# Optimization experiments

Hardware: AMD Instinct MI355X
Metric: run time of the kernel (lower is better)

Reference implementation:

```python
import jax, jax.numpy as jnp
import numpy as np

HID = 1024
HEADS = 16
HEAD_DIM = HID // HEADS
PF = 4096
EPS = 1e-5


def _linear_params(key, d_in, d_out):
    kw, kb = jax.random.split(key)
    bound = 1.0 / np.sqrt(d_in)
    W = jax.random.uniform(kw, (d_in, d_out), jnp.float32, -bound, bound)
    b = jax.random.uniform(kb, (d_out,), jnp.float32, -bound, bound)
    return W, b


def setup_inputs() -> dict:
    key = jax.random.key(0)
    ks = jax.random.split(key, 8)
    src = jax.random.normal(ks[0], (4, 2048, HID), jnp.float32)
    src_mask = jnp.ones((4, 1, 1, 2048), jnp.int32)
    Wq, bq = _linear_params(ks[1], HID, HID)
    Wk, bk = _linear_params(ks[2], HID, HID)
    Wv, bv = _linear_params(ks[3], HID, HID)
    Wo, bo = _linear_params(ks[4], HID, HID)
    W1, b1 = _linear_params(ks[5], HID, PF)
    W2, b2 = _linear_params(ks[6], PF, HID)
    ln1_g = jnp.ones((HID,), jnp.float32); ln1_b = jnp.zeros((HID,), jnp.float32)
    ln2_g = jnp.ones((HID,), jnp.float32); ln2_b = jnp.zeros((HID,), jnp.float32)
    return dict(src=src, src_mask=src_mask, Wq=Wq, bq=bq, Wk=Wk, bk=bk,
                Wv=Wv, bv=bv, Wo=Wo, bo=bo, W1=W1, b1=b1, W2=W2, b2=b2,
                ln1_g=ln1_g, ln1_b=ln1_b, ln2_g=ln2_g, ln2_b=ln2_b)


def _layernorm(x, g, b):
    mu = jnp.mean(x, axis=-1, keepdims=True)
    var = jnp.mean(jnp.square(x - mu), axis=-1, keepdims=True)
    return (x - mu) * jax.lax.rsqrt(var + EPS) * g + b


def _forward(src, src_mask, Wq, bq, Wk, bk, Wv, bv, Wo, bo,
             W1, b1, W2, b2, ln1_g, ln1_b, ln2_g, ln2_b):
    B, S, _ = src.shape
    # multi-head attention
    Q = (src @ Wq + bq).reshape(B, S, HEADS, HEAD_DIM)
    K = (src @ Wk + bk).reshape(B, S, HEADS, HEAD_DIM)
    V = (src @ Wv + bv).reshape(B, S, HEADS, HEAD_DIM)
    scale = np.sqrt(HEAD_DIM).astype(np.float32)
    energy = jnp.einsum('bqnh,bknh->bnqk', Q, K) / scale
    energy = jnp.where(src_mask == 0, jnp.float32(-1e10), energy)
    attn = jax.nn.softmax(energy, axis=-1)
    x = jnp.einsum('bnqk,bknh->bqnh', attn, V).reshape(B, S, HID)
    x = x @ Wo + bo
    src = _layernorm(src + x, ln1_g, ln1_b)
    # feedforward (swish)
    h = src @ W1 + b1
    h = h * jax.nn.sigmoid(h)
    h = h @ W2 + b2
    return _layernorm(src + h, ln2_g, ln2_b)


def reference(src, src_mask, Wq, bq, Wk, bk, Wv, bv, Wo, bo,
              W1, b1, W2, b2, ln1_g, ln1_b, ln2_g, ln2_b):
    return _forward(src, src_mask, Wq, bq, Wk, bk, Wv, bv, Wo, bo,
                    W1, b1, W2, b2, ln1_g, ln1_b, ln2_g, ln2_b)
```

## Files before the change

kernel.cpp:

```cpp
#include <hip/hip_runtime.h>
#include <stdint.h>


typedef __bf16 bf16;
typedef __bf16 bf16x4 __attribute__((ext_vector_type(4)));
typedef __bf16 bf16x8 __attribute__((ext_vector_type(8)));
typedef float  f32x4  __attribute__((ext_vector_type(4)));

__device__ __forceinline__ bf16 f2b(float x){
  uint32_t u = __builtin_bit_cast(uint32_t, x);
  uint32_t r = (u + 0x7FFFu + ((u >> 16) & 1u)) >> 16;
  return __builtin_bit_cast(bf16, (uint16_t)r);
}

__device__ __forceinline__ float ex2(float x){
#if __has_builtin(__builtin_amdgcn_exp2f)
  return __builtin_amdgcn_exp2f(x);
#else
  return __exp2f(x);
#endif
}

__device__ __forceinline__ void gload_lds16(const void* g, void* l){
  __builtin_amdgcn_global_load_lds(
      (const __attribute__((address_space(1))) void*)g,
      (__attribute__((address_space(3))) void*)l, 16, 0, 0);
}

__global__ __launch_bounds__(256) void prep_kernel(
    const float* __restrict__ src, bf16* __restrict__ srcb,
    const float* __restrict__ Wq, const float* __restrict__ Wk,
    const float* __restrict__ Wv, const float* __restrict__ Wo,
    const float* __restrict__ W1, const float* __restrict__ W2,
    bf16* __restrict__ Wqkvt, bf16* __restrict__ Wot,
    bf16* __restrict__ W1t,  bf16* __restrict__ W2t)
{
  __shared__ float t[32][33];
  const int bb = blockIdx.x, tid = threadIdx.x;
  if (bb < 8192){
    const int i = bb*256 + tid;
    const float4 v = ((const float4*)src)[i];
    bf16x4 u = { f2b(v.x), f2b(v.y), f2b(v.z), f2b(v.w) };
    *(bf16x4*)(srcb + (size_t)i*4) = u;
    return;
  }
  const int idx = bb - 8192;
  const float* W; bf16* Wt; int K, N, bx, by;
  if (idx < 3072){
    const int r = idx >> 10, j = idx & 1023;
    W = (r==0)?Wq:(r==1)?Wk:Wv; Wt = Wqkvt + (size_t)r*1024*1024;
    K = 1024; N = 1024; bx = j & 31; by = j >> 5;
  } else if (idx < 4096){
    const int j = idx - 3072;
    W = Wo; Wt = Wot; K = 1024; N = 1024; bx = j & 31; by = j >> 5;
  } else if (idx < 8192){
    const int j = idx - 4096;
    W = W1; Wt = W1t; K = 1024; N = 4096; bx = j & 127; by = j >> 7;
  } else {
    const int j = idx - 8192;
    W = W2; Wt = W2t; K = 4096; N = 1024; bx = j & 31; by = j >> 5;
  }
  const int x = tid & 31, y = tid >> 5;
  const int n0 = bx*32, k0 = by*32;
  #pragma unroll
  for (int r=0;r<4;r++) t[y+8*r][x] = W[(size_t)(k0+y+8*r)*N + n0+x];
  __syncthreads();
  #pragma unroll
  for (int r=0;r<4;r++) Wt[(size_t)(n0+y+8*r)*K + k0+x] = f2b(t[x][y+8*r]);
}

template<int OMODE, int REMAP>
__global__ __launch_bounds__(256) void gemm_bt_kernel(
    const bf16* __restrict__ A, const bf16* __restrict__ Bt,
    const float* __restrict__ bias, void* __restrict__ C,
    int M, int N, int K, float oscale,
    const float* __restrict__ bias2, const float* __restrict__ bias3,
    void* __restrict__ C2, void* __restrict__ C3)
{
  __shared__ bf16 As[2][128*64];
  __shared__ bf16 Bs[2][128*64];
  const int tid = threadIdx.x;
  const int w = tid >> 6, lane = tid & 63;
  const int wr = w >> 1, wc = w & 1;
  const int g16 = lane >> 4, l16 = lane & 15;

  const int nbx = N >> 7;
  const int nby = M >> 7;
  const int lin = blockIdx.x;
  int bx, by;
  if constexpr (REMAP==1){
    const int xcd = lin & 7;
    const int j   = lin >> 3;
    by = xcd * (nby >> 3) + (j / nbx);
    bx = j % nbx;
  } else {
    bx = lin % nbx;
    by = lin / nbx;
  }
  const int m0 = by*128, n0 = bx*128;

  const int srow  = tid >> 3;
  const int sslot = ((tid & 7) ^ (srow & 7)) * 8;
  const bf16* gA = A  + (size_t)(m0 + srow)*K + sslot;
  const bf16* gB = Bt + (size_t)(n0 + srow)*K + sslot;

  f32x4 acc[4][4];
  const f32x4 fz = {0.f,0.f,0.f,0.f};
  #pragma unroll
  for (int m=0;m<4;m++)
    #pragma unroll
    for (int n=0;n<4;n++) acc[m][n] = fz;

  bf16x8 ra[4], rb[4];
  #pragma unroll
  for (int k=0;k<4;k++){
    ra[k] = *(const bf16x8*)(gA + (size_t)(32*k)*K);
    rb[k] = *(const bf16x8*)(gB + (size_t)(32*k)*K);
  }
  asm volatile("s_waitcnt vmcnt(0)" ::: "memory");
  #pragma unroll
  for (int k=0;k<4;k++){
    *(bf16x8*)&As[0][(tid + 256*k)*8] = ra[k];
    *(bf16x8*)&Bs[0][(tid + 256*k)*8] = rb[k];
  }
  const int NT = K >> 6;
  if (NT > 1){
    #pragma unroll
    for (int k=0;k<4;k++){
      ra[k] = *(const bf16x8*)(gA + (size_t)(32*k)*K + 64);
      rb[k] = *(const bf16x8*)(gB + (size_t)(32*k)*K + 64);
    }
  }

  const int l7 = l16 & 7;
  for (int t = 0; t < NT; ++t){
    asm volatile("s_waitcnt lgkmcnt(0)" ::: "memory");
    __builtin_amdgcn_s_barrier();
    asm volatile("" ::: "memory");

    const bf16* as = &As[t&1][0];
    const bf16* bs = &Bs[t&1][0];
    bf16x8 af[2][4], bfv[2][4];
    #pragma unroll
    for (int kk=0;kk<2;kk++){
      #pragma unroll
      for (int m=0;m<4;m++){
        const int r = wr*64 + m*16 + l16;
        af[kk][m] = *(const bf16x8*)&as[r*64 + ((((kk<<2)+g16) ^ l7)<<3)];
      }
      #pragma unroll
      for (int n=0;n<4;n++){
        const int r = wc*64 + n*16 + l16;
        bfv[kk][n] = *(const bf16x8*)&bs[r*64 + ((((kk<<2)+g16) ^ l7)<<3)];
      }
    }
    if (t+1 < NT){
      asm volatile("s_waitcnt vmcnt(0)" ::: "memory");
      bf16* aw = &As[(t+1)&1][0];
      bf16* bw = &Bs[(t+1)&1][0];
      #pragma unroll
      for (int k=0;k<4;k++){
        *(bf16x8*)&aw[(tid + 256*k)*8] = ra[k];
        *(bf16x8*)&bw[(tid + 256*k)*8] = rb[k];
      }
      if (t+2 < NT){
        #pragma unroll
        for (int k=0;k<4;k++){
          ra[k] = *(const bf16x8*)(gA + (size_t)(32*k)*K + (t+2)*64);
          rb[k] = *(const bf16x8*)(gB + (size_t)(32*k)*K + (t+2)*64);
        }
      }
    }
    #pragma unroll
    for (int kk=0;kk<2;kk++)
      #pragma unroll
      for (int m=0;m<4;m++)
        #pragma unroll
        for (int n=0;n<4;n++)
          acc[m][n] = __builtin_amdgcn_mfma_f32_16x16x32_bf16(
              af[kk][m], bfv[kk][n], acc[m][n], 0, 0, 0);
  }

  const int cb = n0 + wc*64 + l16;
  if constexpr (OMODE==4){
    const int region = n0 >> 10;
    const float* bs2 = (region==0)? bias : (region==1)? bias2 : bias3;
    const int colbase = region << 10;
    #pragma unroll
    for (int n=0;n<4;n++){
      const int cl = cb + n*16 - colbase;
      const float bv = bs2[cl];
      #pragma unroll
      for (int m=0;m<4;m++){
        const int rbase = m0 + wr*64 + m*16 + g16*4;
        if (region==2){
          const size_t bq = (size_t)rbase >> 11;
          const int s  = rbase & 2047;
          const int s6 = s & 63;
          const int sp = (s & ~63) | (s6 & 32) | ((s6 & 12) << 1)
                       | ((s6 & 16) >> 2);
          bf16x4 v4 = { f2b(acc[m][n][0] + bv), f2b(acc[m][n][1] + bv),
                        f2b(acc[m][n][2] + bv), f2b(acc[m][n][3] + bv) };
          *(bf16x4*)&((bf16*)C3)[(bq*1024 + (size_t)cl)*2048 + sp] = v4;
        } else {
          #pragma unroll
          for (int r=0;r<4;r++){
            const float v = acc[m][n][r] + bv;
            const size_t row = (size_t)(rbase + r);
            if (region==0) ((bf16*)C )[row*1024 + cl] = f2b(v * oscale);
            else           ((bf16*)C2)[row*1024 + cl] = f2b(v);
          }
        }
      }
    }
  } else {
    #pragma unroll
    for (int n=0;n<4;n++){
      const int col = cb + n*16;
      const float bv = bias[col];
      #pragma unroll
      for (int m=0;m<4;m++){
        const int rbase = m0 + wr*64 + m*16 + g16*4;
        #pragma unroll
        for (int r=0;r<4;r++){
          float v = acc[m][n][r] + bv;
          const size_t row = (size_t)(rbase + r);
          if constexpr (OMODE==0){
            ((float*)C)[row*N + col] = v;
          } else if constexpr (OMODE==1){
            ((bf16*)C)[row*N + col] = f2b(v * oscale);
          } else {
            v = v / (1.f + __expf(-v));
            ((bf16*)C)[row*N + col] = f2b(v);
          }
        }
      }
    }
  }
}

__global__ __launch_bounds__(512) void attn_kernel(
    const bf16* __restrict__ Q, const bf16* __restrict__ Km,
    const bf16* __restrict__ Vt, const int* __restrict__ msk,
    bf16* __restrict__ O)
{
  __shared__ bf16 Ks[3][64*64];
  __shared__ bf16 Vs[3][64*64];
  __shared__ int  Mflag[32];

  const int tid = threadIdx.x;
  const int w = tid>>6, lane = tid&63;
  const int g16 = lane>>4, l16 = lane&15;
  const int lin = blockIdx.x;
  const int xcd = lin & 7, idx = lin >> 3;
  const int bh  = xcd*8 + (idx >> 3);
  const int qt  = idx & 7;
  const int b = bh >> 4, h = bh & 15;
  const int q0 = qt*256 + w*32;

  const bf16* Kb = Km + (size_t)b*2048*1024 + h*64;
  const bf16* Vb = Vt + (size_t)(b*16 + h)*64*2048;
  const int*  mb = msk + b*2048;

  if (tid < 32) Mflag[tid] = 1;

  const int srow = w*8 + (lane>>3);
  const int sslot = ((lane&7) ^ (lane>>3)) * 8;
  const bf16* gK0 = Kb + (size_t)srow*1024 + sslot;
  const bf16* gV0 = Vb + (size_t)srow*2048 + sslot;

  auto stage = [&](int buf, int kv0){
    gload_lds16(gK0 + (size_t)kv0*1024, &Ks[buf][w*512]);
    gload_lds16(gV0 + kv0,              &Vs[buf][w*512]);
  };

  bf16x8 qf[2][2];
  #pragma unroll
  for (int qg=0;qg<2;qg++){
    const bf16* qp = Q + (size_t)(b*2048 + q0 + qg*16 + l16)*1024 + h*64 + g16*8;
    qf[qg][0] = *(const bf16x8*)qp;
    qf[qg][1] = *(const bf16x8*)(qp + 32);
  }

  __syncthreads();
  {
    const int4 a = *(const int4*)(mb + tid*4);
    const bool ok = a.x && a.y && a.z && a.w;
    if (!ok) atomicAnd(&Mflag[tid>>4], 0);
  }
  stage(0, 0);
  stage(1, 64);
  __syncthreads();

  const int l7 = l16 & 7;
  const int kOff0 = l16*64 + ((g16     ^ l7) << 3);
  const int kOff1 = l16*64 + (((4+g16) ^ l7) << 3);

  bf16x8 ones8;
  #pragma unroll
  for (int j=0;j<8;j++) ones8[j] = (bf16)1.0f;

  const f32x4 fz = {0.f,0.f,0.f,0.f};
  f32x4 xa[2][4];
  f32x4 lacc[2] = {fz, fz};
  #pragma unroll
  for (int qg=0;qg<2;qg++)
    #pragma unroll
    for (int jd=0;jd<4;jd++) xa[qg][jd] = fz;

  int cur = 0;
  for (int it = 0; it < 32; ++it){
    const int kv0 = it*64;
    const bf16* ksb = &Ks[cur][0];
    const bf16* vsb = &Vs[cur][0];

    bf16x8 kk[4][2];
    #pragma unroll
    for (int t=0;t<4;t++){
      kk[t][0] = *(const bf16x8*)(ksb + t*1024 + kOff0);
      kk[t][1] = *(const bf16x8*)(ksb + t*1024 + kOff1);
    }
    bf16x8 vw[2][4];
    #pragma unroll
    for (int jd=0;jd<4;jd++){
      vw[0][jd] = *(const bf16x8*)(vsb + jd*1024 + kOff0);
      vw[1][jd] = *(const bf16x8*)(vsb + jd*1024 + kOff1);
    }

    if (it < 30){
      const int pb = (cur >= 1) ? cur-1 : 2;
      stage(pb, kv0 + 128);
    }
    if (it < 30)       asm volatile("s_waitcnt vmcnt(2)" ::: "memory");
    else if (it == 30) asm volatile("s_waitcnt vmcnt(0)" ::: "memory");
    asm volatile("s_waitcnt lgkmcnt(0)" ::: "memory");
    if (it < 31){
      asm volatile("" ::: "memory");
      __builtin_amdgcn_s_barrier();
      asm volatile("" ::: "memory");
    }

    f32x4 st[2][4];
    __builtin_amdgcn_s_setprio(1);
    #pragma unroll
    for (int qg=0;qg<2;qg++){
      #pragma unroll
      for (int t=0;t<4;t++){
        f32x4 a = fz;
        a = __builtin_amdgcn_mfma_f32_16x16x32_bf16(kk[t][0], qf[qg][0], a, 0,0,0);
        a = __builtin_amdgcn_mfma_f32_16x16x32_bf16(kk[t][1], qf[qg][1], a, 0,0,0);
        st[qg][t] = a;
      }
    }
    __builtin_amdgcn_s_setprio(0);

    if (!Mflag[it]){
      int4 mm[4];
      #pragma unroll
      for (int t=0;t<4;t++) mm[t] = *(const int4*)(mb + kv0 + t*16 + 4*g16);
      #pragma unroll
      for (int qg=0;qg<2;qg++)
        #pragma unroll
        for (int t=0;t<4;t++){
          st[qg][t][0] = (mm[t].x==0) ? -1e9f : st[qg][t][0];
          st[qg][t][1] = (mm[t].y==0) ? -1e9f : st[qg][t][1];
          st[qg][t][2] = (mm[t].z==0) ? -1e9f : st[qg][t][2];
          st[qg][t][3] = (mm[t].w==0) ? -1e9f : st[qg][t][3];
        }
    }

    bf16x8 pw[2][2];
    #pragma unroll
    for (int qg=0;qg<2;qg++){
      #pragma unroll
      for (int t=0;t<4;t++){
        const int hb = (t&1)*4;
        pw[qg][t>>1][hb+0] = (bf16)ex2(st[qg][t][0]);
        pw[qg][t>>1][hb+1] = (bf16)ex2(st[qg][t][1]);
        pw[qg][t>>1][hb+2] = (bf16)ex2(st[qg][t][2]);
        pw[qg][t>>1][hb+3] = (bf16)ex2(st[qg][t][3]);
      }
    }
    __builtin_amdgcn_s_setprio(1);
    #pragma unroll
    for (int w2=0;w2<2;w2++){
      #pragma unroll
      for (int jd=0;jd<4;jd++){
        xa[0][jd] = __builtin_amdgcn_mfma_f32_16x16x32_bf16(vw[w2][jd], pw[0][w2], xa[0][jd], 0,0,0);
        xa[1][jd] = __builtin_amdgcn_mfma_f32_16x16x32_bf16(vw[w2][jd], pw[1][w2], xa[1][jd], 0,0,0);
      }
      lacc[0] = __builtin_amdgcn_mfma_f32_16x16x32_bf16(ones8, pw[0][w2], lacc[0], 0,0,0);
      lacc[1] = __builtin_amdgcn_mfma_f32_16x16x32_bf16(ones8, pw[1][w2], lacc[1], 0,0,0);
    }
    __builtin_amdgcn_s_setprio(0);

    cur = (cur==2) ? 0 : cur+1;
  }

  #pragma unroll
  for (int qg=0;qg<2;qg++){
    const float rl = 1.f / lacc[qg][0];
    const size_t row = (size_t)(b*2048 + q0 + qg*16 + l16);
    #pragma unroll
    for (int jd=0;jd<4;jd++){
      bf16x4 ov = { f2b(xa[qg][jd][0]*rl), f2b(xa[qg][jd][1]*rl),
                    f2b(xa[qg][jd][2]*rl), f2b(xa[qg][jd][3]*rl) };
      *(bf16x4*)(O + row*1024 + h*64 + jd*16 + 4*g16) = ov;
    }
  }
}

template<int RBF>
__global__ __launch_bounds__(256) void addln_kernel(
    const bf16* __restrict__ X, const void* __restrict__ R,
    const float* __restrict__ g, const float* __restrict__ be,
    float* __restrict__ of, bf16* __restrict__ ob)
{
  const int row = blockIdx.x, tid = threadIdx.x;
  const bf16x4 vxb = *(const bf16x4*)(X + (size_t)row*1024 + tid*4);
  float r0, r1, r2, r3;
  if constexpr (RBF==1){
    const bf16x4 vrb = *(const bf16x4*)((const bf16*)R + (size_t)row*1024 + tid*4);
    r0 = (float)vrb[0]; r1 = (float)vrb[1]; r2 = (float)vrb[2]; r3 = (float)vrb[3];
  } else {
    const float4 vr = ((const float4*)((const float*)R + (size_t)row*1024))[tid];
    r0 = vr.x; r1 = vr.y; r2 = vr.z; r3 = vr.w;
  }
  const float a0 = (float)vxb[0]+r0, a1 = (float)vxb[1]+r1;
  const float a2 = (float)vxb[2]+r2, a3 = (float)vxb[3]+r3;
  float s = a0+a1+a2+a3;
  float q = a0*a0 + a1*a1 + a2*a2 + a3*a3;
  #pragma unroll
  for (int off=1; off<64; off<<=1){
    s += __shfl_xor(s, off, 64);
    q += __shfl_xor(q, off, 64);
  }
  __shared__ float sb[8];
  if ((tid&63)==0){ sb[tid>>6] = s; sb[4+(tid>>6)] = q; }
  __syncthreads();
  s = sb[0]+sb[1]+sb[2]+sb[3];
  q = sb[4]+sb[5]+sb[6]+sb[7];
  const float mu = s*(1.f/1024.f);
  const float rs = rsqrtf(q*(1.f/1024.f) - mu*mu + 1e-5f);
  const float4 gg = ((const float4*)g)[tid];
  const float4 bb = ((const float4*)be)[tid];
  const float o0 = (a0-mu)*rs*gg.x + bb.x;
  const float o1 = (a1-mu)*rs*gg.y + bb.y;
  const float o2 = (a2-mu)*rs*gg.z + bb.z;
  const float o3 = (a3-mu)*rs*gg.w + bb.w;
  if (of){
    float4 o; o.x=o0; o.y=o1; o.z=o2; o.w=o3;
    ((float4*)(of + (size_t)row*1024))[tid] = o;
  }
  if (ob){
    bf16x4 u = { f2b(o0), f2b(o1), f2b(o2), f2b(o3) };
    *(bf16x4*)(ob + (size_t)row*1024 + tid*4) = u;
  }
}

extern "C" void kernel_launch(void* const* d_in, const int* in_sizes, int n_in,
                              void* d_out, int out_size, void* d_ws, size_t ws_size,
                              hipStream_t stream)
{
  const float* src  = (const float*)d_in[0];
  const int*   mask = (const int*)  d_in[1];
  const float* Wq = (const float*)d_in[2];  const float* bq = (const float*)d_in[3];
  const float* Wk = (const float*)d_in[4];  const float* bk = (const float*)d_in[5];
  const float* Wv = (const float*)d_in[6];  const float* bv = (const float*)d_in[7];
  const float* Wo = (const float*)d_in[8];  const float* bo = (const float*)d_in[9];
  const float* W1 = (const float*)d_in[10]; const float* b1 = (const float*)d_in[11];
  const float* W2 = (const float*)d_in[12]; const float* b2 = (const float*)d_in[13];
  const float* g1 = (const float*)d_in[14]; const float* be1 = (const float*)d_in[15];
  const float* g2 = (const float*)d_in[16]; const float* be2 = (const float*)d_in[17];

  char* ws = (char*)d_ws;
  const size_t MB = 1u<<20;
  bf16* srcb  = (bf16*)(ws + 0*MB);
  bf16* Wqkvt = (bf16*)(ws + 16*MB);
  bf16* Wot   = (bf16*)(ws + 22*MB);
  bf16* W1t   = (bf16*)(ws + 24*MB);
  bf16* W2t   = (bf16*)(ws + 32*MB);
  bf16* Qb    = (bf16*)(ws + 40*MB);
  bf16* Kb    = (bf16*)(ws + 56*MB);
  bf16* Vtb   = (bf16*)(ws + 72*MB);
  bf16* AO    = (bf16*)(ws + 88*MB);
  bf16*  X1   = (bf16*)(ws + 40*MB);
  bf16*  S1B  = (bf16*)(ws + 72*MB);
  bf16*  H1   = (bf16*)(ws + 104*MB);
  bf16*  F2   = (bf16*)(ws + 40*MB);

  const float QSC = 0.18033688011112042f;

  prep_kernel<<<20480, 256, 0, stream>>>(src, srcb, Wq, Wk, Wv, Wo, W1, W2,
                                         Wqkvt, Wot, W1t, W2t);

  gemm_bt_kernel<4,0><<<24*64, 256, 0, stream>>>(
      srcb, Wqkvt, bq, Qb, 8192, 3072, 1024, QSC, bk, bv, Kb, Vtb);

  attn_kernel<<<512, 512, 0, stream>>>(Qb, Kb, Vtb, mask, AO);

  gemm_bt_kernel<1,1><<<8*64,  256, 0, stream>>>(
      AO, Wot, bo, X1, 8192, 1024, 1024, 1.f, nullptr, nullptr, nullptr, nullptr);
  addln_kernel<0><<<8192, 256, 0, stream>>>(X1, src, g1, be1,
                                            (float*)nullptr, S1B);

  gemm_bt_kernel<2,0><<<32*64, 256, 0, stream>>>(
      S1B, W1t, b1, H1, 8192, 4096, 1024, 1.f, nullptr, nullptr, nullptr, nullptr);
  gemm_bt_kernel<1,1><<<8*64,  256, 0, stream>>>(
      H1,  W2t, b2, F2, 8192, 1024, 4096, 1.f, nullptr, nullptr, nullptr, nullptr);
  addln_kernel<1><<<8192, 256, 0, stream>>>(F2, S1B, g2, be2,
                                            (float*)d_out, (bf16*)nullptr);
}
```

Baseline: 368.1 us.

## Halve attention block warps, give each warp 64 query rows

The attention kernel now launches 256 threads per block instead of 512. Each of the 4 warps handles 64 query rows (four 16-row groups) instead of 32, and the K/V staging and mask-flag logic are adjusted so each thread issues twice as many loads. The aim is to reuse every K/V fragment read from LDS across more query rows and to cut per-block barrier and staging overhead. The cost is higher register pressure from the larger accumulators and less latency hiding, since fewer waves run per block.

```diff
diff --git a/kernel.cpp b/kernel.cpp
--- a/kernel.cpp
+++ b/kernel.cpp
@@ -239,7 +239,7 @@
   }
 }
 
-__global__ __launch_bounds__(512) void attn_kernel(
+__global__ __launch_bounds__(256) void attn_kernel(
     const bf16* __restrict__ Q, const bf16* __restrict__ Km,
     const bf16* __restrict__ Vt, const int* __restrict__ msk,
     bf16* __restrict__ O)
@@ -256,7 +256,7 @@
   const int bh  = xcd*8 + (idx >> 3);
   const int qt  = idx & 7;
   const int b = bh >> 4, h = bh & 15;
-  const int q0 = qt*256 + w*32;
+  const int q0 = qt*256 + w*64;
 
   const bf16* Kb = Km + (size_t)b*2048*1024 + h*64;
   const bf16* Vb = Vt + (size_t)(b*16 + h)*64*2048;
@@ -264,19 +264,23 @@
 
   if (tid < 32) Mflag[tid] = 1;
 
-  const int srow = w*8 + (lane>>3);
+  const int srow = w*16 + (lane>>3);
   const int sslot = ((lane&7) ^ (lane>>3)) * 8;
   const bf16* gK0 = Kb + (size_t)srow*1024 + sslot;
   const bf16* gV0 = Vb + (size_t)srow*2048 + sslot;
 
   auto stage = [&](int buf, int kv0){
-    gload_lds16(gK0 + (size_t)kv0*1024, &Ks[buf][w*512]);
-    gload_lds16(gV0 + kv0,              &Vs[buf][w*512]);
+    bf16* kl = &Ks[buf][w*1024];
+    bf16* vl = &Vs[buf][w*1024];
+    gload_lds16(gK0 + (size_t)kv0*1024, kl);
+    gload_lds16(gK0 + (size_t)(kv0+8)*1024, kl + 512);
+    gload_lds16(gV0 + kv0,      vl);
+    gload_lds16(gV0 + kv0 + 8,  vl + 512);
   };
 
-  bf16x8 qf[2][2];
-  #pragma unroll
-  for (int qg=0;qg<2;qg++){
+  bf16x8 qf[4][2];
+  #pragma unroll
+  for (int qg=0;qg<4;qg++){
     const bf16* qp = Q + (size_t)(b*2048 + q0 + qg*16 + l16)*1024 + h*64 + g16*8;
     qf[qg][0] = *(const bf16x8*)qp;
     qf[qg][1] = *(const bf16x8*)(qp + 32);
@@ -284,9 +288,10 @@
 
   __syncthreads();
   {
-    const int4 a = *(const int4*)(mb + tid*4);
-    const bool ok = a.x && a.y && a.z && a.w;
-    if (!ok) atomicAnd(&Mflag[tid>>4], 0);
+    const int4 a = *(const int4*)(mb + tid*8);
+    const int4 c = *(const int4*)(mb + tid*8 + 4);
+    const bool ok = a.x && a.y && a.z && a.w && c.x && c.y && c.z && c.w;
+    if (!ok) atomicAnd(&Mflag[tid>>3], 0);
   }
   stage(0, 0);
   stage(1, 64);
@@ -301,10 +306,10 @@
   for (int j=0;j<8;j++) ones8[j] = (bf16)1.0f;
 
   const f32x4 fz = {0.f,0.f,0.f,0.f};
-  f32x4 xa[2][4];
-  f32x4 lacc[2] = {fz, fz};
-  #pragma unroll
-  for (int qg=0;qg<2;qg++)
+  f32x4 xa[4][4];
+  f32x4 lacc[4] = {fz, fz, fz, fz};
+  #pragma unroll
+  for (int qg=0;qg<4;qg++)
     #pragma unroll
     for (int jd=0;jd<4;jd++) xa[qg][jd] = fz;
 
@@ -331,7 +336,7 @@
       const int pb = (cur >= 1) ? cur-1 : 2;
       stage(pb, kv0 + 128);
     }
-    if (it < 30)       asm volatile("s_waitcnt vmcnt(2)" ::: "memory");
+    if (it < 30)       asm volatile("s_waitcnt vmcnt(4)" ::: "memory");
     else if (it == 30) asm volatile("s_waitcnt vmcnt(0)" ::: "memory");
     asm volatile("s_waitcnt lgkmcnt(0)" ::: "memory");
     if (it < 31){
@@ -340,57 +345,54 @@
       asm volatile("" ::: "memory");
     }
 
-    f32x4 st[2][4];
-    __builtin_amdgcn_s_setprio(1);
-    #pragma unroll
-    for (int qg=0;qg<2;qg++){
+    const bool needmask = !Mflag[it];
+    int4 mm[4];
+    if (needmask){
+      #pragma unroll
+      for (int t=0;t<4;t++) mm[t] = *(const int4*)(mb + kv0 + t*16 + 4*g16);
+    }
+
+    bf16x8 pw[4][2];
+    #pragma unroll
+    for (int qg=0;qg<4;qg++){
+      f32x4 st[4];
+      __builtin_amdgcn_s_setprio(1);
       #pragma unroll
       for (int t=0;t<4;t++){
         f32x4 a = fz;
         a = __builtin_amdgcn_mfma_f32_16x16x32_bf16(kk[t][0], qf[qg][0], a, 0,0,0);
         a = __builtin_amdgcn_mfma_f32_16x16x32_bf16(kk[t][1], qf[qg][1], a, 0,0,0);
-        st[qg][t] = a;
-      }
-    }
-    __builtin_amdgcn_s_setprio(0);
-
-    if (!Mflag[it]){
-      int4 mm[4];
-      #pragma unroll
-      for (int t=0;t<4;t++) mm[t] = *(const int4*)(mb + kv0 + t*16 + 4*g16);
-      #pragma unroll
-      for (int qg=0;qg<2;qg++)
+        st[t] = a;
+      }
+      __builtin_amdgcn_s_setprio(0);
+      if (needmask){
         #pragma unroll
         for (int t=0;t<4;t++){
-          st[qg][t][0] = (mm[t].x==0) ? -1e9f : st[qg][t][0];
-          st[qg][t][1] = (mm[t].y==0) ? -1e9f : st[qg][t][1];
-          st[qg][t][2] = (mm[t].z==0) ? -1e9f : st[qg][t][2];
-          st[qg][t][3] = (mm[t].w==0) ? -1e9f : st[qg][t][3];
+          st[t][0] = (mm[t].x==0) ? -1e9f : st[t][0];
+          st[t][1] = (mm[t].y==0) ? -1e9f : st[t][1];
+          st[t][2] = (mm[t].z==0) ? -1e9f : st[t][2];
+          st[t][3] = (mm[t].w==0) ? -1e9f : st[t][3];
         }
-    }
-
-    bf16x8 pw[2][2];
-    #pragma unroll
-    for (int qg=0;qg<2;qg++){
+      }
       #pragma unroll
       for (int t=0;t<4;t++){
         const int hb = (t&1)*4;
-        pw[qg][t>>1][hb+0] = (bf16)ex2(st[qg][t][0]);
-        pw[qg][t>>1][hb+1] = (bf16)ex2(st[qg][t][1]);
-        pw[qg][t>>1][hb+2] = (bf16)ex2(st[qg][t][2]);
-        pw[qg][t>>1][hb+3] = (bf16)ex2(st[qg][t][3]);
+        pw[qg][t>>1][hb+0] = (bf16)ex2(st[t][0]);
+        pw[qg][t>>1][hb+1] = (bf16)ex2(st[t][1]);
+        pw[qg][t>>1][hb+2] = (bf16)ex2(st[t][2]);
+        pw[qg][t>>1][hb+3] = (bf16)ex2(st[t][3]);
       }
     }
     __builtin_amdgcn_s_setprio(1);
     #pragma unroll
     for (int w2=0;w2<2;w2++){
       #pragma unroll
-      for (int jd=0;jd<4;jd++){
-        xa[0][jd] = __builtin_amdgcn_mfma_f32_16x16x32_bf16(vw[w2][jd], pw[0][w2], xa[0][jd], 0,0,0);
-        xa[1][jd] = __builtin_amdgcn_mfma_f32_16x16x32_bf16(vw[w2][jd], pw[1][w2], xa[1][jd], 0,0,0);
-      }
-      lacc[0] = __builtin_amdgcn_mfma_f32_16x16x32_bf16(ones8, pw[0][w2], lacc[0], 0,0,0);
-      lacc[1] = __builtin_amdgcn_mfma_f32_16x16x32_bf16(ones8, pw[1][w2], lacc[1], 0,0,0);
+      for (int qg=0;qg<4;qg++){
+        #pragma unroll
+        for (int jd=0;jd<4;jd++)
+          xa[qg][jd] = __builtin_amdgcn_mfma_f32_16x16x32_bf16(vw[w2][jd], pw[qg][w2], xa[qg][jd], 0,0,0);
+        lacc[qg] = __builtin_amdgcn_mfma_f32_16x16x32_bf16(ones8, pw[qg][w2], lacc[qg], 0,0,0);
+      }
     }
     __builtin_amdgcn_s_setprio(0);
 
@@ -398,7 +400,7 @@
   }
 
   #pragma unroll
-  for (int qg=0;qg<2;qg++){
+  for (int qg=0;qg<4;qg++){
     const float rl = 1.f / lacc[qg][0];
     const size_t row = (size_t)(b*2048 + q0 + qg*16 + l16);
     #pragma unroll
@@ -497,7 +499,7 @@
   gemm_bt_kernel<4,0><<<24*64, 256, 0, stream>>>(
       srcb, Wqkvt, bq, Qb, 8192, 3072, 1024, QSC, bk, bv, Kb, Vtb);
 
-  attn_kernel<<<512, 512, 0, stream>>>(Qb, Kb, Vtb, mask, AO);
+  attn_kernel<<<512, 256, 0, stream>>>(Qb, Kb, Vtb, mask, AO);
 
   gemm_bt_kernel<1,1><<<8*64,  256, 0, stream>>>(
       AO, Wot, bo, X1, 8192, 1024, 1024, 1.f, nullptr, nullptr, nullptr, nullptr);
```

Measured after the change: 390.7 us. 6.1% more time.
